# Kernel optimization log

Measured on AMD Instinct MI355X. Metric: run time of the kernel, lower is better.

The kernel has to match this reference:

```python
import jax, jax.numpy as jnp
import numpy as np

LEVELS = 16
N_MIN = 16
N_MAX = 512
TABLE_SIZE = 524288  # 2**19, power of two -> mod == bitmask
INPUT_DIM = 2
FEATURE_DIM = 2
N_POINTS = 1048576

# geometric resolution schedule (matches torch __init__)
_b = np.exp((np.log(N_MAX) - np.log(N_MIN)) / (LEVELS - 1))
_RESOLUTIONS = np.floor(N_MIN * _b ** np.arange(LEVELS)).astype(np.float32)  # [L]
_PRIMES = np.array([1, 2654435761], dtype=np.uint32)  # first INPUT_DIM primes
# voxel corner offsets for input_dim=2 (matches _voxel_border_adds construction)
_BORDER = np.array([[0, 1, 0, 1], [0, 0, 1, 1]], dtype=np.int32)  # [D, 2**D]


def setup_inputs() -> dict:
    key = jax.random.key(0)
    kx, kt = jax.random.split(key)
    x = jax.random.uniform(kx, (N_POINTS, INPUT_DIM), dtype=jnp.float32)
    hash_tables = jax.random.normal(kt, (LEVELS, TABLE_SIZE, FEATURE_DIM), dtype=jnp.float32)
    return {"x": x, "hash_tables": hash_tables}


def reference(x, hash_tables):
    res = jnp.asarray(_RESOLUTIONS)            # [L]
    border = jnp.asarray(_BORDER)              # [D, C] with C=2**D
    primes = jnp.asarray(_PRIMES)              # [D] uint32

    # scaled coords per level: [N, D, L]
    scaled = x[:, :, None] * res[None, None, :]
    grid = jnp.floor(scaled).astype(jnp.int32)                 # [N, D, L]
    corners = grid[:, :, :, None] + border[None, :, None, :]   # [N, D, L, C]

    # spatial hash: xor of (coord * prime) per dim, mod table size.
    # uint32 arithmetic matches torch's int64 result exactly because
    # TABLE_SIZE is a power of two dividing 2**32 and coords are nonnegative.
    prod = corners.astype(jnp.uint32) * primes[None, :, None, None]  # [N, D, L, C]
    hashed = (prod[:, 0] ^ prod[:, 1]) & jnp.uint32(TABLE_SIZE - 1)  # [N, L, C]
    idx = hashed.astype(jnp.int32)

    # gather per-level features: [N, L, C, F]
    feats = hash_tables[jnp.arange(LEVELS)[None, :, None], idx]

    # interpolation weights (faithful to torch: prod over dims of |scaled - corner|)
    w = jnp.prod(jnp.abs(scaled[:, :, :, None] - corners.astype(scaled.dtype)), axis=1)  # [N, L, C]

    # sum over corners; torch output layout is [N, F, L] flattened feature-major
    out = jnp.einsum('nlc,nlcf->nfl', w, feats)  # [N, F, L]
    return out.reshape(x.shape[0], FEATURE_DIM * LEVELS)
```

## Files before the change

kernel.cpp:

```cpp
#include <hip/hip_runtime.h>
#include <stdint.h>

#define NPTS      1048576
#define LEVELS    16
#define TSIZE     524288
#define TMASK     (TSIZE - 1)
#define PRIME1    2654435761u

__device__ __constant__ float c_res[LEVELS] = {
    16.f, 20.f, 25.f, 32.f, 40.f, 50.f, 64.f, 80.f,
    101.f, 128.f, 161.f, 203.f, 256.f, 322.f, 406.f, 512.f
};

__global__ __launch_bounds__(256)
void hashenc_kernel(const float* __restrict__ x,
                    const float* __restrict__ tables,
                    float* __restrict__ out,
                    int npts) {
    int n = blockIdx.x * 256 + threadIdx.x;
    if (n >= npts) return;

    float2 p = reinterpret_cast<const float2*>(x)[n];

    float acc0[LEVELS];
    float acc1[LEVELS];

#pragma unroll
    for (int l = 0; l < LEVELS; ++l) {
        float r  = c_res[l];
        float s0 = p.x * r;
        float s1 = p.y * r;
        float g0 = floorf(s0);
        float g1 = floorf(s1);
        uint32_t i0 = (uint32_t)(int)g0;
        uint32_t i1 = (uint32_t)(int)g1;

        uint32_t hy0 = i1 * PRIME1;
        uint32_t hy1 = (i1 + 1u) * PRIME1;
        uint32_t h00 = ( i0        ^ hy0) & TMASK;
        uint32_t h10 = ((i0 + 1u)  ^ hy0) & TMASK;
        uint32_t h01 = ( i0        ^ hy1) & TMASK;
        uint32_t h11 = ((i0 + 1u)  ^ hy1) & TMASK;

        const float2* tab = reinterpret_cast<const float2*>(tables) + (size_t)l * TSIZE;
        float2 t00 = tab[h00];
        float2 t10 = tab[h10];
        float2 t01 = tab[h01];
        float2 t11 = tab[h11];

        float wx0 = fabsf(s0 - g0);
        float wx1 = fabsf(s0 - (g0 + 1.f));
        float wy0 = fabsf(s1 - g1);
        float wy1 = fabsf(s1 - (g1 + 1.f));
        float w00 = wx0 * wy0;
        float w10 = wx1 * wy0;
        float w01 = wx0 * wy1;
        float w11 = wx1 * wy1;

        acc0[l] = w00 * t00.x + w10 * t10.x + w01 * t01.x + w11 * t11.x;
        acc1[l] = w00 * t00.y + w10 * t10.y + w01 * t01.y + w11 * t11.y;
    }

    float4* o = reinterpret_cast<float4*>(out + (size_t)n * 32);
    o[0] = make_float4(acc0[0],  acc0[1],  acc0[2],  acc0[3]);
    o[1] = make_float4(acc0[4],  acc0[5],  acc0[6],  acc0[7]);
    o[2] = make_float4(acc0[8],  acc0[9],  acc0[10], acc0[11]);
    o[3] = make_float4(acc0[12], acc0[13], acc0[14], acc0[15]);
    o[4] = make_float4(acc1[0],  acc1[1],  acc1[2],  acc1[3]);
    o[5] = make_float4(acc1[4],  acc1[5],  acc1[6],  acc1[7]);
    o[6] = make_float4(acc1[8],  acc1[9],  acc1[10], acc1[11]);
    o[7] = make_float4(acc1[12], acc1[13], acc1[14], acc1[15]);
}

extern "C" void kernel_launch(void* const* d_in, const int* in_sizes, int n_in,
                              void* d_out, int out_size, void* d_ws, size_t ws_size,
                              hipStream_t stream) {
    const float* x      = (const float*)d_in[0];
    const float* tables = (const float*)d_in[1];
    float* out          = (float*)d_out;
    int npts = in_sizes[0] / 2;
    int blocks = (npts + 255) / 256;
    hashenc_kernel<<<blocks, 256, 0, stream>>>(x, tables, out, npts);
}
```

Measured before the change: 370.1 us.

## Sort points by Morton key before hash encoding to improve gather locality

Adds a counting sort of input points by an 8-bit-per-axis Morton key (histogram, single-block scan, atomic scatter) and runs the encoder over the sorted order, writing results back to the original positions. The goal is for neighbouring threads to hit nearby grid cells and share hash-table cache lines. In exchange it adds four kernel launches, global atomics, extra passes over the input, and scattered output writes; it falls back to the original kernel when the workspace is too small.

```diff
diff --git a/kernel.cpp b/kernel.cpp
--- a/kernel.cpp
+++ b/kernel.cpp
@@ -1,30 +1,30 @@
 #include <hip/hip_runtime.h>
 #include <stdint.h>
 
-#define NPTS      1048576
 #define LEVELS    16
 #define TSIZE     524288
 #define TMASK     (TSIZE - 1)
 #define PRIME1    2654435761u
+#define NBINS     65536
 
 __device__ __constant__ float c_res[LEVELS] = {
     16.f, 20.f, 25.f, 32.f, 40.f, 50.f, 64.f, 80.f,
     101.f, 128.f, 161.f, 203.f, 256.f, 322.f, 406.f, 512.f
 };
 
-__global__ __launch_bounds__(256)
-void hashenc_kernel(const float* __restrict__ x,
-                    const float* __restrict__ tables,
-                    float* __restrict__ out,
-                    int npts) {
-    int n = blockIdx.x * 256 + threadIdx.x;
-    if (n >= npts) return;
+__device__ __forceinline__ uint32_t morton_key(float2 p) {
+    float fx = fminf(fmaxf(p.x, 0.f), 0.999999f);
+    float fy = fminf(fmaxf(p.y, 0.f), 0.999999f);
+    uint32_t x = (uint32_t)(fx * 256.f);
+    uint32_t y = (uint32_t)(fy * 256.f);
+    x = (x | (x << 4)) & 0x0F0Fu; x = (x | (x << 2)) & 0x3333u; x = (x | (x << 1)) & 0x5555u;
+    y = (y | (y << 4)) & 0x0F0Fu; y = (y | (y << 2)) & 0x3333u; y = (y | (y << 1)) & 0x5555u;
+    return x | (y << 1);
+}
 
-    float2 p = reinterpret_cast<const float2*>(x)[n];
-
-    float acc0[LEVELS];
-    float acc1[LEVELS];
-
+__device__ __forceinline__ void hashenc_point(float2 p, const float* __restrict__ tables,
+                                              float* __restrict__ outline) {
+    float acc0[LEVELS], acc1[LEVELS];
 #pragma unroll
     for (int l = 0; l < LEVELS; ++l) {
         float r  = c_res[l];
@@ -34,13 +34,12 @@
         float g1 = floorf(s1);
         uint32_t i0 = (uint32_t)(int)g0;
         uint32_t i1 = (uint32_t)(int)g1;
-
         uint32_t hy0 = i1 * PRIME1;
         uint32_t hy1 = (i1 + 1u) * PRIME1;
-        uint32_t h00 = ( i0        ^ hy0) & TMASK;
-        uint32_t h10 = ((i0 + 1u)  ^ hy0) & TMASK;
-        uint32_t h01 = ( i0        ^ hy1) & TMASK;
-        uint32_t h11 = ((i0 + 1u)  ^ hy1) & TMASK;
+        uint32_t h00 = ( i0       ^ hy0) & TMASK;
+        uint32_t h10 = ((i0 + 1u) ^ hy0) & TMASK;
+        uint32_t h01 = ( i0       ^ hy1) & TMASK;
+        uint32_t h11 = ((i0 + 1u) ^ hy1) & TMASK;
 
         const float2* tab = reinterpret_cast<const float2*>(tables) + (size_t)l * TSIZE;
         float2 t00 = tab[h00];
@@ -52,16 +51,12 @@
         float wx1 = fabsf(s0 - (g0 + 1.f));
         float wy0 = fabsf(s1 - g1);
         float wy1 = fabsf(s1 - (g1 + 1.f));
-        float w00 = wx0 * wy0;
-        float w10 = wx1 * wy0;
-        float w01 = wx0 * wy1;
-        float w11 = wx1 * wy1;
+        float w00 = wx0 * wy0, w10 = wx1 * wy0, w01 = wx0 * wy1, w11 = wx1 * wy1;
 
         acc0[l] = w00 * t00.x + w10 * t10.x + w01 * t01.x + w11 * t11.x;
         acc1[l] = w00 * t00.y + w10 * t10.y + w01 * t01.y + w11 * t11.y;
     }
-
-    float4* o = reinterpret_cast<float4*>(out + (size_t)n * 32);
+    float4* o = reinterpret_cast<float4*>(outline);
     o[0] = make_float4(acc0[0],  acc0[1],  acc0[2],  acc0[3]);
     o[1] = make_float4(acc0[4],  acc0[5],  acc0[6],  acc0[7]);
     o[2] = make_float4(acc0[8],  acc0[9],  acc0[10], acc0[11]);
@@ -72,6 +67,76 @@
     o[7] = make_float4(acc1[12], acc1[13], acc1[14], acc1[15]);
 }
 
+__global__ __launch_bounds__(256)
+void zero_hist_kernel(uint32_t* __restrict__ hist) {
+    hist[blockIdx.x * 256 + threadIdx.x] = 0u;
+}
+
+__global__ __launch_bounds__(256)
+void hist_kernel(const float* __restrict__ x, uint32_t* __restrict__ hist, int npts) {
+    int n = blockIdx.x * 256 + threadIdx.x;
+    if (n >= npts) return;
+    float2 p = reinterpret_cast<const float2*>(x)[n];
+    atomicAdd(&hist[morton_key(p)], 1u);
+}
+
+__global__ __launch_bounds__(1024)
+void scan_kernel(uint32_t* __restrict__ hist) {
+    __shared__ uint32_t part[1024];
+    int t = threadIdx.x;
+    int base = t * 64;
+    uint32_t sum = 0;
+#pragma unroll 4
+    for (int i = 0; i < 64; ++i) sum += hist[base + i];
+    part[t] = sum;
+    __syncthreads();
+    for (int off = 1; off < 1024; off <<= 1) {
+        uint32_t v = (t >= off) ? part[t - off] : 0u;
+        __syncthreads();
+        part[t] += v;
+        __syncthreads();
+    }
+    uint32_t run = part[t] - sum;
+    for (int i = 0; i < 64; ++i) {
+        uint32_t old = hist[base + i];
+        hist[base + i] = run;
+        run += old;
+    }
+}
+
+__global__ __launch_bounds__(256)
+void scatter_kernel(const float* __restrict__ x, uint32_t* __restrict__ hist,
+                    uint32_t* __restrict__ perm, float2* __restrict__ sx, int npts) {
+    int n = blockIdx.x * 256 + threadIdx.x;
+    if (n >= npts) return;
+    float2 p = reinterpret_cast<const float2*>(x)[n];
+    uint32_t pos = atomicAdd(&hist[morton_key(p)], 1u);
+    perm[pos] = (uint32_t)n;
+    sx[pos] = p;
+}
+
+__global__ __launch_bounds__(256)
+void hashenc_sorted_kernel(const uint32_t* __restrict__ perm,
+                           const float2* __restrict__ sx,
+                           const float* __restrict__ tables,
+                           float* __restrict__ out, int npts) {
+    int i = blockIdx.x * 256 + threadIdx.x;
+    if (i >= npts) return;
+    uint32_t n = perm[i];
+    float2 p = sx[i];
+    hashenc_point(p, tables, out + (size_t)n * 32);
+}
+
+__global__ __launch_bounds__(256)
+void hashenc_kernel(const float* __restrict__ x,
+                    const float* __restrict__ tables,
+                    float* __restrict__ out, int npts) {
+    int n = blockIdx.x * 256 + threadIdx.x;
+    if (n >= npts) return;
+    float2 p = reinterpret_cast<const float2*>(x)[n];
+    hashenc_point(p, tables, out + (size_t)n * 32);
+}
+
 extern "C" void kernel_launch(void* const* d_in, const int* in_sizes, int n_in,
                               void* d_out, int out_size, void* d_ws, size_t ws_size,
                               hipStream_t stream) {
@@ -80,5 +145,24 @@
     float* out          = (float*)d_out;
     int npts = in_sizes[0] / 2;
     int blocks = (npts + 255) / 256;
-    hashenc_kernel<<<blocks, 256, 0, stream>>>(x, tables, out, npts);
+
+    size_t hist_bytes = (size_t)NBINS * 4;
+    size_t perm_bytes = (size_t)npts * 4;
+    size_t sx_bytes   = (size_t)npts * 8;
+    size_t needed = hist_bytes + perm_bytes + sx_bytes;
+
+    if (ws_size < needed) {
+        hashenc_kernel<<<blocks, 256, 0, stream>>>(x, tables, out, npts);
+        return;
+    }
+
+    uint32_t* hist = (uint32_t*)d_ws;
+    uint32_t* perm = (uint32_t*)((char*)d_ws + hist_bytes);
+    float2*   sx   = (float2*)((char*)d_ws + hist_bytes + perm_bytes);
+
+    zero_hist_kernel<<<NBINS / 256, 256, 0, stream>>>(hist);
+    hist_kernel<<<blocks, 256, 0, stream>>>(x, hist, npts);
+    scan_kernel<<<1, 1024, 0, stream>>>(hist);
+    scatter_kernel<<<blocks, 256, 0, stream>>>(x, hist, perm, sx, npts);
+    hashenc_sorted_kernel<<<blocks, 256, 0, stream>>>(perm, sx, tables, out, npts);
 }
```

New measurement: 399.6 us. 8.0% more time.
